# Performance work log

Measured on AMD Instinct MI355X. Metric: run time of the kernel, lower is better.

## Reference

```python
import jax, jax.numpy as jnp
import numpy as np

ASPECT_RATIOS = jnp.array([0.5, 1.0, 2.0], dtype=jnp.float32)
SCALES = jnp.array([1.0, 2.0, 4.0, 8.0, 16.0], dtype=jnp.float32)
BASE_SIZE = 16
STRIDE = 16
NEG_OVERLAP = 0.3
POS_OVERLAP = 0.7
PADDING = 0.0
RPN_BATCH = 256
RPN_FG_FRACTION = 0.5


def _mkanchors(ws, hs, x_ctr, y_ctr):
    return jnp.stack([x_ctr - 0.5 * (ws - 1), y_ctr - 0.5 * (hs - 1),
                      x_ctr + 0.5 * (ws - 1), y_ctr + 0.5 * (hs - 1)], axis=-1)


def _base_anchors():
    w = h = float(BASE_SIZE)
    x_ctr = y_ctr = 0.5 * (BASE_SIZE - 1)
    size = w * h
    size_ratios = size / ASPECT_RATIOS
    ws = jnp.round(jnp.sqrt(size_ratios))
    hs = jnp.round(ws * ASPECT_RATIOS)
    ratio_anchors = _mkanchors(ws, hs, x_ctr, y_ctr)          # (R,4)
    rw = ratio_anchors[:, 2] - ratio_anchors[:, 0] + 1
    rh = ratio_anchors[:, 3] - ratio_anchors[:, 1] + 1
    rx = ratio_anchors[:, 0] + 0.5 * (rw - 1)
    ry = ratio_anchors[:, 1] + 0.5 * (rh - 1)
    ws2 = rw[:, None] * SCALES[None, :]                        # (R,S)
    hs2 = rh[:, None] * SCALES[None, :]
    anchors = _mkanchors(ws2, hs2, rx[:, None], ry[:, None])   # (R,S,4)
    return anchors.reshape(-1, 4)                              # (A=R*S,4)


def _shifted_anchors(r, c):
    base = _base_anchors()                                     # (A,4)
    sx = jnp.arange(c, dtype=jnp.float32) * STRIDE
    sy = jnp.arange(r, dtype=jnp.float32) * STRIDE
    SX, SY = jnp.meshgrid(sx, sy)                              # (r,c)
    shifts = jnp.stack([SX.ravel(), SY.ravel(), SX.ravel(), SY.ravel()], axis=1)
    return (shifts[:, None, :] + base[None, :, :]).reshape(-1, 4)  # (K=r*c*A,4)


def _iou(a, b):
    area_a = (a[:, 2] - a[:, 0] + 1) * (a[:, 3] - a[:, 1] + 1)
    area_b = (b[:, 2] - b[:, 0] + 1) * (b[:, 3] - b[:, 1] + 1)
    iw = jnp.minimum(a[:, None, 2], b[None, :, 2]) - jnp.maximum(a[:, None, 0], b[None, :, 0]) + 1
    ih = jnp.minimum(a[:, None, 3], b[None, :, 3]) - jnp.maximum(a[:, None, 1], b[None, :, 1]) + 1
    inter = jnp.maximum(iw, 0) * jnp.maximum(ih, 0)
    return inter / (area_a[:, None] + area_b[None, :] - inter)


def _bbox_transform(ex, gt):
    ew = ex[:, 2] - ex[:, 0] + 1.0
    eh = ex[:, 3] - ex[:, 1] + 1.0
    ecx = ex[:, 0] + 0.5 * ew
    ecy = ex[:, 1] + 0.5 * eh
    gw = gt[:, 2] - gt[:, 0] + 1.0
    gh = gt[:, 3] - gt[:, 1] + 1.0
    gcx = gt[:, 0] + 0.5 * gw
    gcy = gt[:, 1] + 0.5 * gh
    return jnp.stack([(gcx - ecx) / ew, (gcy - ecy) / eh,
                      jnp.log(gw / ew), jnp.log(gh / eh)], axis=1)


def reference(target_bounding_boxes, metadata, scores):
    meta = metadata[0]
    gt = target_bounding_boxes[0]                               # (G,4)
    r, c = scores.shape[1], scores.shape[2]
    anchors = _shifted_anchors(r, c)                            # (K,4)
    K = anchors.shape[0]
    h, w = meta[0], meta[1]

    # anchors fully inside the image (padding=0); outside anchors masked
    inside = ((anchors[:, 0] >= -PADDING) & (anchors[:, 1] >= -PADDING) &
              (anchors[:, 2] < w + PADDING) & (anchors[:, 3] < h + PADDING))

    clipped = jnp.stack([jnp.clip(anchors[:, 0], 0.0, w - 1),
                         jnp.clip(anchors[:, 1], 0.0, h - 1),
                         jnp.clip(anchors[:, 2], 0.0, w - 1),
                         jnp.clip(anchors[:, 3], 0.0, h - 1)], axis=1)

    overlaps = _iou(clipped, gt)                                # (K,G)
    overlaps = jnp.where(inside[:, None], overlaps, -1.0)       # ignore outside anchors
    argmax_overlaps = jnp.argmax(overlaps, axis=1)              # best gt per anchor
    max_overlaps = jnp.max(overlaps, axis=1)
    gt_argmax = jnp.argmax(overlaps, axis=0)                    # best anchor per gt

    labels = jnp.full((K,), -1.0, dtype=jnp.float32)
    labels = jnp.where(inside & (max_overlaps < NEG_OVERLAP), 0.0, labels)
    labels = labels.at[gt_argmax].set(1.0)                      # dedup handled by .set
    labels = jnp.where(inside & (max_overlaps >= POS_OVERLAP), 1.0, labels)
    labels = jnp.where(inside, labels, -1.0)                    # unmap fill=-1

    # deterministic subsampling (original shuffles randomly): keep first-by-index
    num_fg = int(RPN_FG_FRACTION * RPN_BATCH)
    pos = labels == 1.0
    pos_rank = jnp.cumsum(pos.astype(jnp.int32))
    labels = jnp.where(pos & (pos_rank > num_fg), -1.0, labels)
    num_pos = jnp.minimum(pos.sum(), num_fg)
    num_bg = RPN_BATCH - num_pos
    neg = labels == 0.0
    neg_rank = jnp.cumsum(neg.astype(jnp.int32))
    labels = jnp.where(neg & (neg_rank > num_bg), -1.0, labels)

    matched_gt = gt[argmax_overlaps]                            # (K,4) gather
    bbox_targets = _bbox_transform(clipped, matched_gt)
    bbox_targets = jnp.where(inside[:, None], bbox_targets, 0.0)  # unmap fill=0

    return anchors[None], bbox_targets[None], labels[None]


def setup_inputs() -> dict:
    key = jax.random.key(0)
    k1, k2 = jax.random.split(key)
    H = W = 1600
    G = 100
    r = c = H // STRIDE                                          # 100
    A = 15                                                       # 3 ratios * 5 scales
    xy = jax.random.uniform(k1, (G, 2), minval=0.0, maxval=1400.0)
    wh = jax.random.uniform(k2, (G, 2), minval=16.0, maxval=200.0)
    gt = jnp.concatenate([xy, xy + wh], axis=1)[None]            # (1,G,4)
    metadata = jnp.array([[float(H), float(W), 1.0]], dtype=jnp.float32)
    scores = jnp.zeros((1, r, c, A), dtype=jnp.float32)          # only shape is used
    return {"target_bounding_boxes": gt, "metadata": metadata, "scores": scores}
```

## Files before the change

kernel.cpp:

```cpp
#include <hip/hip_runtime.h>
#include <math.h>


#define NUM_A 15
#define NUM_FG 128
#define RPN_BATCH 256
#define BLOCK 256
#define MAXG 256
#define MAXNB 1024
#define FIXT 1024

#define EXT_X1 (-176.f)
#define EXT_X2 (191.f)
#define EXT_Y1 (-168.f)
#define EXT_Y2 (183.f)

__device__ __forceinline__ void base_anchor(int a, float& bx1, float& by1,
                                            float& bx2, float& by2) {
    const float RW[3] = {23.f, 16.f, 11.f};
    const float RH[3] = {12.f, 16.f, 22.f};
    int i = a / 5;
    int j = a - i * 5;
    float sc = (float)(1 << j);
    float w = RW[i] * sc;
    float h = RH[i] * sc;
    bx1 = 7.5f - 0.5f * (w - 1.f);
    by1 = 7.5f - 0.5f * (h - 1.f);
    bx2 = 7.5f + 0.5f * (w - 1.f);
    by2 = 7.5f + 0.5f * (h - 1.f);
}

__device__ __forceinline__ void anchor_coords(int k, int c, float& x1, float& y1,
                                              float& x2, float& y2) {
    int a = k % NUM_A;
    int p = k / NUM_A;
    int xi = p % c;
    int yi = p / c;
    float bx1, by1, bx2, by2;
    base_anchor(a, bx1, by1, bx2, by2);
    float sx = (float)xi * 16.f;
    float sy = (float)yi * 16.f;
    x1 = sx + bx1;  y1 = sy + by1;
    x2 = sx + bx2;  y2 = sy + by2;
}

__device__ __forceinline__ unsigned long long packvk(float v, int k) {
    unsigned u = __float_as_uint(v);
    u = (u & 0x80000000u) ? ~u : (u | 0x80000000u);
    return ((unsigned long long)u << 32) | (unsigned)(~k);
}

__global__ void __launch_bounds__(BLOCK) k_main(
        const float* __restrict__ gt, const float* __restrict__ meta,
        float* __restrict__ out_anch, float* __restrict__ out_bb,
        float* __restrict__ out_lab,
        unsigned long long* __restrict__ pbm, unsigned long long* __restrict__ nbm,
        unsigned long long* __restrict__ bestg, int K, int c, int G) {
    __shared__ float4 s_gt[MAXG];
    __shared__ float4 s_gtc[MAXG];
    __shared__ int s_gidx[MAXG];
    __shared__ unsigned long long s_best[MAXG];
    __shared__ int s_nl;
    int tid = threadIdx.x;
    int lane = tid & 63, wid = tid >> 6;
    const float4* gtv = (const float4*)gt;

    float h = meta[0], w = meta[1];
    float wm1 = __fsub_rn(w, 1.f), hm1 = __fsub_rn(h, 1.f);

    int k0 = blockIdx.x * BLOCK;
    int k1 = min(k0 + BLOCK - 1, K - 1);
    int p0 = k0 / NUM_A, p1 = k1 / NUM_A;
    int y0 = p0 / c, y1 = p1 / c;
    int xm0, xm1;
    if (y0 == y1) { xm0 = p0 - y0 * c; xm1 = p1 - y1 * c; }
    else          { xm0 = 0;           xm1 = c - 1; }
    float bbx1 = fminf(fmaxf((float)(xm0 * 16) + EXT_X1, 0.f), wm1);
    float bbx2 = fminf(fmaxf((float)(xm1 * 16) + EXT_X2, 0.f), wm1);
    float bby1 = fminf(fmaxf((float)(y0 * 16) + EXT_Y1, 0.f), hm1);
    float bby2 = fminf(fmaxf((float)(y1 * 16) + EXT_Y2, 0.f), hm1);

    if (tid == 0) s_nl = 0;
    for (int g = tid; g < G; g += BLOCK) s_best[g] = 0ULL;
    __syncthreads();
    for (int g = tid; g < G; g += BLOCK) {
        float4 gb = gtv[g];
        s_gt[g] = gb;
        float ox = __fadd_rn(__fsub_rn(fminf(bbx2, gb.z), fmaxf(bbx1, gb.x)), 1.f);
        float oy = __fadd_rn(__fsub_rn(fminf(bby2, gb.w), fmaxf(bby1, gb.y)), 1.f);
        if (ox > 0.f && oy > 0.f) {
            int slot = atomicAdd(&s_nl, 1);
            s_gtc[slot] = gb;
            s_gidx[slot] = g;
        }
    }
    __syncthreads();
    int NL = s_nl;

    int k = blockIdx.x * BLOCK + tid;
    bool valid = (k < K);

    float x1, y1f, x2, y2f;
    anchor_coords(k, c, x1, y1f, x2, y2f);
    if (valid) ((float4*)out_anch)[k] = make_float4(x1, y1f, x2, y2f);
    bool inside = (x1 >= 0.f) && (y1f >= 0.f) && (x2 < w) && (y2f < h);
    bool act_anchor = valid && inside;

    float cx1 = fminf(fmaxf(x1, 0.f), wm1);
    float cy1 = fminf(fmaxf(y1f, 0.f), hm1);
    float cx2 = fminf(fmaxf(x2, 0.f), wm1);
    float cy2 = fminf(fmaxf(y2f, 0.f), hm1);
    float area_a = __fmul_rn(__fadd_rn(__fsub_rn(cx2, cx1), 1.f),
                             __fadd_rn(__fsub_rn(cy2, cy1), 1.f));

    float maxv = 0.f;
    int arg = 0;
    if (act_anchor) {
        for (int i = 0; i < NL; ++i) {
            float4 gb = s_gtc[i];
            int g = s_gidx[i];
            float gw = __fadd_rn(__fsub_rn(gb.z, gb.x), 1.f);
            float gh = __fadd_rn(__fsub_rn(gb.w, gb.y), 1.f);
            float areab = __fmul_rn(gw, gh);
            float iw = __fadd_rn(__fsub_rn(fminf(cx2, gb.z), fmaxf(cx1, gb.x)), 1.f);
            float ih = __fadd_rn(__fsub_rn(fminf(cy2, gb.w), fmaxf(cy1, gb.y)), 1.f);
            float inter = __fmul_rn(fmaxf(iw, 0.f), fmaxf(ih, 0.f));
            if (inter > 0.f) {
                float denom = __fsub_rn(__fadd_rn(area_a, areab), inter);
                float v = __fdiv_rn(inter, denom);
                atomicMax(&s_best[g], packvk(v, k));
                if (v > maxv || (v == maxv && g < arg)) { maxv = v; arg = g; }
            }
        }
    }
    __syncthreads();
    for (int g = tid; g < G; g += BLOCK)
        if (s_best[g] != 0ULL) atomicMax(&bestg[g], s_best[g]);

    float labf = -1.f;
    if (valid) {
        float t0 = 0.f, t1 = 0.f, t2 = 0.f, t3 = 0.f;
        if (inside) {
            labf = (maxv >= 0.7f) ? 1.f : (maxv < 0.3f ? 0.f : -1.f);
            float4 gb = s_gt[arg];
            float ew  = __fadd_rn(__fsub_rn(cx2, cx1), 1.f);
            float eh  = __fadd_rn(__fsub_rn(cy2, cy1), 1.f);
            float ecx = __fadd_rn(cx1, __fmul_rn(0.5f, ew));
            float ecy = __fadd_rn(cy1, __fmul_rn(0.5f, eh));
            float gw  = __fadd_rn(__fsub_rn(gb.z, gb.x), 1.f);
            float gh  = __fadd_rn(__fsub_rn(gb.w, gb.y), 1.f);
            float gcx = __fadd_rn(gb.x, __fmul_rn(0.5f, gw));
            float gcy = __fadd_rn(gb.y, __fmul_rn(0.5f, gh));
            t0 = __fdiv_rn(__fsub_rn(gcx, ecx), ew);
            t1 = __fdiv_rn(__fsub_rn(gcy, ecy), eh);
            t2 = logf(__fdiv_rn(gw, ew));
            t3 = logf(__fdiv_rn(gh, eh));
        }
        ((float4*)out_bb)[k] = make_float4(t0, t1, t2, t3);
        out_lab[k] = -1.f;
    }

    bool pos = valid && (labf == 1.f);
    bool neg = valid && (labf == 0.f);
    unsigned long long bp = __ballot(pos ? 1 : 0);
    unsigned long long bn = __ballot(neg ? 1 : 0);
    if (lane == 0) {
        pbm[blockIdx.x * 4 + wid] = bp;
        nbm[blockIdx.x * 4 + wid] = bn;
    }
}

__global__ void __launch_bounds__(FIXT) k_fix(
        float* __restrict__ out_lab,
        const unsigned long long* __restrict__ pbm,
        const unsigned long long* __restrict__ nbm,
        const unsigned long long* __restrict__ bestg, int K, int NB, int G) {
    __shared__ int s_p[FIXT], s_n[FIXT];
    __shared__ int s_k[MAXG];
    __shared__ unsigned long long cmask[MAXNB][4];
    int t = threadIdx.x;

    cmask[t][0] = 0ULL; cmask[t][1] = 0ULL;
    cmask[t][2] = 0ULL; cmask[t][3] = 0ULL;

    int cp = 0, cn = 0;
    if (t < NB) {
        const unsigned long long* pp = pbm + 4 * t;
        const unsigned long long* nn = nbm + 4 * t;
        cp = __popcll(pp[0]) + __popcll(pp[1]) + __popcll(pp[2]) + __popcll(pp[3]);
        cn = __popcll(nn[0]) + __popcll(nn[1]) + __popcll(nn[2]) + __popcll(nn[3]);
    }
    s_p[t] = cp;
    s_n[t] = cn;

    int kstar = -1;
    if (t < G) {
        unsigned long long u = bestg[t];
        if (u != 0ULL)
            kstar = (int)(~(unsigned)(u & 0xffffffffu));
    }
    if (t < MAXG) s_k[t] = kstar;
    __syncthreads();
    bool mine = (kstar >= 0);
    if (mine) {
        for (int j = 0; j < t; ++j)
            if (s_k[j] == kstar) { mine = false; break; }
    }
    if (mine) {
        int b = kstar >> 8;
        int bit = kstar & 255;
        unsigned long long msk = 1ULL << (bit & 63);
        unsigned long long pw = pbm[b * 4 + (bit >> 6)];
        unsigned long long nw = nbm[b * 4 + (bit >> 6)];
        bool was1 = (pw & msk) != 0ULL;
        bool was0 = (nw & msk) != 0ULL;
        if (!was1) {
            atomicAdd(&s_p[b], 1);
            if (was0) atomicAdd(&s_n[b], -1);
        }
        atomicOr(&cmask[b][bit >> 6], msk);
    }
    __syncthreads();

    int op = s_p[t], on = s_n[t];
    int vp = op, vn = on;
    for (int off = 1; off < FIXT; off <<= 1) {
        int ap = 0, an = 0;
        if (t >= off) { ap = s_p[t - off]; an = s_n[t - off]; }
        __syncthreads();
        vp += ap; vn += an;
        s_p[t] = vp; s_n[t] = vn;
        __syncthreads();
    }
    int total_pos = s_p[FIXT - 1];
    int np = total_pos < NUM_FG ? total_pos : NUM_FG;
    int nbg = RPN_BATCH - np;
    int ep = vp - op, en = vn - on;

    if (t < NB) {
        int base_k = t * BLOCK;
        if (ep < NUM_FG && op > 0) {
            int rank = ep;
            for (int wd = 0; wd < 4 && rank < NUM_FG; ++wd) {
                unsigned long long m = pbm[t * 4 + wd] | cmask[t][wd];
                while (m != 0ULL && rank < NUM_FG) {
                    int bit = __builtin_ctzll(m);
                    m &= m - 1ULL;
                    ++rank;
                    out_lab[base_k + wd * 64 + bit] = 1.0f;
                }
            }
        }
        if (en < nbg && on > 0) {
            int rank = en;
            for (int wd = 0; wd < 4 && rank < nbg; ++wd) {
                unsigned long long m = nbm[t * 4 + wd] & ~cmask[t][wd];
                while (m != 0ULL && rank < nbg) {
                    int bit = __builtin_ctzll(m);
                    m &= m - 1ULL;
                    ++rank;
                    out_lab[base_k + wd * 64 + bit] = 0.0f;
                }
            }
        }
    }
}

extern "C" void kernel_launch(void* const* d_in, const int* in_sizes, int n_in,
                              void* d_out, int out_size, void* d_ws, size_t ws_size,
                              hipStream_t stream) {
    const float* gt   = (const float*)d_in[0];
    const float* meta = (const float*)d_in[1];
    int G  = in_sizes[0] / 4;
    int rc = in_sizes[2] / NUM_A;
    int c = 1;
    while ((long long)(c + 1) * (c + 1) <= (long long)rc) ++c;
    int K  = rc * NUM_A;
    int NB = (K + BLOCK - 1) / BLOCK;

    float* out      = (float*)d_out;
    float* out_anch = out;
    float* out_bb   = out + (size_t)4 * K;
    float* out_lab  = out + (size_t)8 * K;

    unsigned long long* bestg = (unsigned long long*)d_ws;
    unsigned long long* pbm   = bestg + MAXG;
    unsigned long long* nbm   = pbm + (size_t)MAXNB * 4;

    hipMemsetAsync(bestg, 0, (size_t)G * sizeof(unsigned long long), stream);
    hipLaunchKernelGGL(k_main, dim3(NB), dim3(BLOCK), 0, stream,
                       gt, meta, out_anch, out_bb, out_lab, pbm, nbm, bestg, K, c, G);
    hipLaunchKernelGGL(k_fix, dim3(1), dim3(FIXT), 0, stream,
                       out_lab, pbm, nbm, bestg, K, NB, G);
}
```

Baseline: 105.0 us.

## Fuse label-fixup kernel into main kernel via last-block completion counter

Merges the single-block fixup kernel into the main kernel. Each block increments a global done counter, and the last block to finish runs the prefix sum and label subsampling with 256 threads, each handling three blocks' bitmasks. This removes one kernel launch and the gap between the two launches, at the cost of extra shared memory in every block and a serial per-thread loop over gt boxes to rebuild the corrected masks.

```diff
diff --git a/kernel.cpp b/kernel.cpp
--- a/kernel.cpp
+++ b/kernel.cpp
@@ -7,8 +7,8 @@
 #define RPN_BATCH 256
 #define BLOCK 256
 #define MAXG 256
-#define MAXNB 1024
-#define FIXT 1024
+#define CPT 3
+#define FIXN (BLOCK * CPT)
 
 #define EXT_X1 (-176.f)
 #define EXT_X2 (191.f)
@@ -50,17 +50,22 @@
     return ((unsigned long long)u << 32) | (unsigned)(~k);
 }
 
-__global__ void __launch_bounds__(BLOCK) k_main(
+__global__ void __launch_bounds__(BLOCK) k_all(
         const float* __restrict__ gt, const float* __restrict__ meta,
         float* __restrict__ out_anch, float* __restrict__ out_bb,
         float* __restrict__ out_lab,
         unsigned long long* __restrict__ pbm, unsigned long long* __restrict__ nbm,
-        unsigned long long* __restrict__ bestg, int K, int c, int G) {
+        unsigned long long* __restrict__ bestg, unsigned int* __restrict__ donecnt,
+        int K, int c, int G, int NB) {
     __shared__ float4 s_gt[MAXG];
     __shared__ float4 s_gtc[MAXG];
     __shared__ int s_gidx[MAXG];
     __shared__ unsigned long long s_best[MAXG];
-    __shared__ int s_nl;
+    __shared__ int s_nl, s_last;
+    __shared__ int s_p[FIXN], s_n[FIXN];
+    __shared__ int s_cp[BLOCK], s_cn[BLOCK];
+    __shared__ int s_k[BLOCK], s_kc[BLOCK];
+
     int tid = threadIdx.x;
     int lane = tid & 63, wid = tid >> 6;
     const float4* gtv = (const float4*)gt;
@@ -70,11 +75,11 @@
 
     int k0 = blockIdx.x * BLOCK;
     int k1 = min(k0 + BLOCK - 1, K - 1);
-    int p0 = k0 / NUM_A, p1 = k1 / NUM_A;
-    int y0 = p0 / c, y1 = p1 / c;
+    int pp0 = k0 / NUM_A, pp1 = k1 / NUM_A;
+    int y0 = pp0 / c, y1 = pp1 / c;
     int xm0, xm1;
-    if (y0 == y1) { xm0 = p0 - y0 * c; xm1 = p1 - y1 * c; }
-    else          { xm0 = 0;           xm1 = c - 1; }
+    if (y0 == y1) { xm0 = pp0 - y0 * c; xm1 = pp1 - y1 * c; }
+    else          { xm0 = 0;            xm1 = c - 1; }
     float bbx1 = fminf(fmaxf((float)(xm0 * 16) + EXT_X1, 0.f), wm1);
     float bbx2 = fminf(fmaxf((float)(xm1 * 16) + EXT_X2, 0.f), wm1);
     float bby1 = fminf(fmaxf((float)(y0 * 16) + EXT_Y1, 0.f), hm1);
@@ -168,38 +173,38 @@
         pbm[blockIdx.x * 4 + wid] = bp;
         nbm[blockIdx.x * 4 + wid] = bn;
     }
-}
-
-__global__ void __launch_bounds__(FIXT) k_fix(
-        float* __restrict__ out_lab,
-        const unsigned long long* __restrict__ pbm,
-        const unsigned long long* __restrict__ nbm,
-        const unsigned long long* __restrict__ bestg, int K, int NB, int G) {
-    __shared__ int s_p[FIXT], s_n[FIXT];
-    __shared__ int s_k[MAXG];
-    __shared__ unsigned long long cmask[MAXNB][4];
-    int t = threadIdx.x;
-
-    cmask[t][0] = 0ULL; cmask[t][1] = 0ULL;
-    cmask[t][2] = 0ULL; cmask[t][3] = 0ULL;
-
-    int cp = 0, cn = 0;
-    if (t < NB) {
-        const unsigned long long* pp = pbm + 4 * t;
-        const unsigned long long* nn = nbm + 4 * t;
-        cp = __popcll(pp[0]) + __popcll(pp[1]) + __popcll(pp[2]) + __popcll(pp[3]);
-        cn = __popcll(nn[0]) + __popcll(nn[1]) + __popcll(nn[2]) + __popcll(nn[3]);
-    }
-    s_p[t] = cp;
-    s_n[t] = cn;
-
+
+    __threadfence();
+    __syncthreads();
+    if (tid == 0) {
+        unsigned int old = __hip_atomic_fetch_add(donecnt, 1u, __ATOMIC_ACQ_REL,
+                                                  __HIP_MEMORY_SCOPE_AGENT);
+        s_last = (old == (unsigned)(NB - 1)) ? 1 : 0;
+    }
+    __syncthreads();
+    if (!s_last) return;
+    __threadfence();
+
+    int t = tid;
+    for (int i = 0; i < CPT; ++i) {
+        int b = t * CPT + i;
+        int cp = 0, cn = 0;
+        if (b < NB) {
+            const unsigned long long* pw = pbm + 4 * b;
+            const unsigned long long* nw = nbm + 4 * b;
+            cp = __popcll(pw[0]) + __popcll(pw[1]) + __popcll(pw[2]) + __popcll(pw[3]);
+            cn = __popcll(nw[0]) + __popcll(nw[1]) + __popcll(nw[2]) + __popcll(nw[3]);
+        }
+        s_p[t * CPT + i] = cp;
+        s_n[t * CPT + i] = cn;
+    }
     int kstar = -1;
     if (t < G) {
         unsigned long long u = bestg[t];
         if (u != 0ULL)
             kstar = (int)(~(unsigned)(u & 0xffffffffu));
     }
-    if (t < MAXG) s_k[t] = kstar;
+    s_k[t] = kstar;
     __syncthreads();
     bool mine = (kstar >= 0);
     if (mine) {
@@ -210,59 +215,73 @@
         int b = kstar >> 8;
         int bit = kstar & 255;
         unsigned long long msk = 1ULL << (bit & 63);
-        unsigned long long pw = pbm[b * 4 + (bit >> 6)];
-        unsigned long long nw = nbm[b * 4 + (bit >> 6)];
-        bool was1 = (pw & msk) != 0ULL;
-        bool was0 = (nw & msk) != 0ULL;
+        bool was1 = (pbm[b * 4 + (bit >> 6)] & msk) != 0ULL;
+        bool was0 = (nbm[b * 4 + (bit >> 6)] & msk) != 0ULL;
         if (!was1) {
             atomicAdd(&s_p[b], 1);
             if (was0) atomicAdd(&s_n[b], -1);
         }
-        atomicOr(&cmask[b][bit >> 6], msk);
-    }
-    __syncthreads();
-
-    int op = s_p[t], on = s_n[t];
+    }
+    s_kc[t] = mine ? kstar : -1;
+    __syncthreads();
+
+    int op = s_p[t * CPT] + s_p[t * CPT + 1] + s_p[t * CPT + 2];
+    int on = s_n[t * CPT] + s_n[t * CPT + 1] + s_n[t * CPT + 2];
+    s_cp[t] = op; s_cn[t] = on;
+    __syncthreads();
     int vp = op, vn = on;
-    for (int off = 1; off < FIXT; off <<= 1) {
+    for (int off = 1; off < BLOCK; off <<= 1) {
         int ap = 0, an = 0;
-        if (t >= off) { ap = s_p[t - off]; an = s_n[t - off]; }
+        if (t >= off) { ap = s_cp[t - off]; an = s_cn[t - off]; }
         __syncthreads();
         vp += ap; vn += an;
-        s_p[t] = vp; s_n[t] = vn;
+        s_cp[t] = vp; s_cn[t] = vn;
         __syncthreads();
     }
-    int total_pos = s_p[FIXT - 1];
+    int total_pos = s_cp[BLOCK - 1];
     int np = total_pos < NUM_FG ? total_pos : NUM_FG;
     int nbg = RPN_BATCH - np;
     int ep = vp - op, en = vn - on;
 
-    if (t < NB) {
-        int base_k = t * BLOCK;
-        if (ep < NUM_FG && op > 0) {
+    for (int i = 0; i < CPT; ++i) {
+        int b = t * CPT + i;
+        if (b >= NB) break;
+        unsigned long long c0 = 0ULL, c1 = 0ULL, c2 = 0ULL, c3 = 0ULL;
+        for (int j = 0; j < G; ++j) {
+            int ks = s_kc[j];
+            bool inb = (ks >= 0) && ((ks >> 8) == b);
+            unsigned long long m = 1ULL << (ks & 63);
+            int wd = (ks >> 6) & 3;
+            c0 |= (inb && wd == 0) ? m : 0ULL;
+            c1 |= (inb && wd == 1) ? m : 0ULL;
+            c2 |= (inb && wd == 2) ? m : 0ULL;
+            c3 |= (inb && wd == 3) ? m : 0ULL;
+        }
+        int bk = b * BLOCK;
+        if (ep < NUM_FG) {
             int rank = ep;
-            for (int wd = 0; wd < 4 && rank < NUM_FG; ++wd) {
-                unsigned long long m = pbm[t * 4 + wd] | cmask[t][wd];
-                while (m != 0ULL && rank < NUM_FG) {
-                    int bit = __builtin_ctzll(m);
-                    m &= m - 1ULL;
-                    ++rank;
-                    out_lab[base_k + wd * 64 + bit] = 1.0f;
-                }
-            }
-        }
-        if (en < nbg && on > 0) {
+            unsigned long long m;
+            #define POSWALK(WD, CW) \
+                m = pbm[b * 4 + WD] | CW; \
+                while (m != 0ULL && rank < NUM_FG) { \
+                    int bt = __builtin_ctzll(m); m &= m - 1ULL; ++rank; \
+                    out_lab[bk + WD * 64 + bt] = 1.0f; }
+            POSWALK(0, c0) POSWALK(1, c1) POSWALK(2, c2) POSWALK(3, c3)
+            #undef POSWALK
+        }
+        if (en < nbg) {
             int rank = en;
-            for (int wd = 0; wd < 4 && rank < nbg; ++wd) {
-                unsigned long long m = nbm[t * 4 + wd] & ~cmask[t][wd];
-                while (m != 0ULL && rank < nbg) {
-                    int bit = __builtin_ctzll(m);
-                    m &= m - 1ULL;
-                    ++rank;
-                    out_lab[base_k + wd * 64 + bit] = 0.0f;
-                }
-            }
-        }
+            unsigned long long m;
+            #define NEGWALK(WD, CW) \
+                m = nbm[b * 4 + WD] & ~CW; \
+                while (m != 0ULL && rank < nbg) { \
+                    int bt = __builtin_ctzll(m); m &= m - 1ULL; ++rank; \
+                    out_lab[bk + WD * 64 + bt] = 0.0f; }
+            NEGWALK(0, c0) NEGWALK(1, c1) NEGWALK(2, c2) NEGWALK(3, c3)
+            #undef NEGWALK
+        }
+        ep += s_p[b];
+        en += s_n[b];
     }
 }
 
@@ -284,12 +303,12 @@
     float* out_lab  = out + (size_t)8 * K;
 
     unsigned long long* bestg = (unsigned long long*)d_ws;
-    unsigned long long* pbm   = bestg + MAXG;
-    unsigned long long* nbm   = pbm + (size_t)MAXNB * 4;
-
-    hipMemsetAsync(bestg, 0, (size_t)G * sizeof(unsigned long long), stream);
-    hipLaunchKernelGGL(k_main, dim3(NB), dim3(BLOCK), 0, stream,
-                       gt, meta, out_anch, out_bb, out_lab, pbm, nbm, bestg, K, c, G);
-    hipLaunchKernelGGL(k_fix, dim3(1), dim3(FIXT), 0, stream,
-                       out_lab, pbm, nbm, bestg, K, NB, G);
-}
+    unsigned int* donecnt = (unsigned int*)(bestg + MAXG);
+    unsigned long long* pbm = (unsigned long long*)(donecnt + 16);
+    unsigned long long* nbm = pbm + (size_t)FIXN * 4;
+
+    hipMemsetAsync(bestg, 0, MAXG * sizeof(unsigned long long) + 64, stream);
+    hipLaunchKernelGGL(k_all, dim3(NB), dim3(BLOCK), 0, stream,
+                       gt, meta, out_anch, out_bb, out_lab, pbm, nbm, bestg,
+                       donecnt, K, c, G, NB);
+}
```

Result: slower. 173.5 us (+65.2%).
